# Kernel optimization log

Measured on AMD Instinct MI355X. Metric: run time of the kernel, lower is better.

The kernel has to match this reference:

```python
import jax, jax.numpy as jnp
import numpy as np

N = 50000
E = 600000
D_IN = 128
D_OUT = 128


def setup_inputs() -> dict:
    key = jax.random.key(0)
    k1, k2, k3 = jax.random.split(key, 3)
    x = jax.random.normal(k1, (N, D_IN), dtype=jnp.float32)
    edge_index = jax.random.randint(k2, (2, E), 0, N, dtype=jnp.int64)
    W = jax.random.normal(k3, (D_IN, D_OUT), dtype=jnp.float32) / np.sqrt(D_IN)
    b = jnp.zeros((D_OUT,), dtype=jnp.float32)
    return {"x": x, "edge_index": edge_index, "W": W, "b": b}


def reference(x, edge_index, W, b):
    n = x.shape[0]
    # add self-loops (PyG GCNConv default add_self_loops=True)
    loop = jnp.arange(n, dtype=edge_index.dtype)
    src = jnp.concatenate([edge_index[0], loop])  # message sources
    dst = jnp.concatenate([edge_index[1], loop])  # aggregation targets

    # linear transform first (small GEMM), then normalized aggregation
    h = x @ W  # [N, D_OUT]

    ones = jnp.ones(src.shape[0], dtype=x.dtype)
    deg = jax.ops.segment_sum(ones, dst, num_segments=n)  # in-degree incl. self-loop
    dis = jnp.where(deg > 0, jax.lax.rsqrt(jnp.maximum(deg, 1.0)), 0.0)
    norm = dis[src] * dis[dst]  # [E+N]

    msg = h[src] * norm[:, None]  # gather + scale, memory-bound
    out = jax.ops.segment_sum(msg, dst, num_segments=n)  # scatter-add
    return out + b
```

## Files before the change

kernel.cpp:

```cpp
#include <hip/hip_runtime.h>

#define D 128
#define CAP 1024
#define NBMAX 1024
#define EPB 4096

typedef short bf16x8 __attribute__((ext_vector_type(8)));
typedef float f32x4 __attribute__((ext_vector_type(4)));

__device__ __forceinline__ unsigned bf16_rne(float f) {
    unsigned u = __float_as_uint(f);
    unsigned r = u + 0x7FFFu + ((u >> 16) & 1u);
    return r >> 16;
}

__device__ __forceinline__ void bf16_split(float f, short& hi, short& lo) {
    unsigned h = bf16_rne(f);
    float hf = __uint_as_float(h << 16);
    hi = (short)h;
    lo = (short)bf16_rne(f - hf);
}

__device__ __forceinline__ unsigned pk2(float lo, float hi) {
    return bf16_rne(lo) | (bf16_rne(hi) << 16);
}

__device__ __forceinline__ float lo16(unsigned u) { return __uint_as_float(u << 16); }
__device__ __forceinline__ float hi16(unsigned u) { return __uint_as_float(u & 0xFFFF0000u); }

__global__ void deg_kernel(const int* __restrict__ ei, int* __restrict__ deg, int E) {
    int e = blockIdx.x * blockDim.x + threadIdx.x;
    if (e < E) atomicAdd(&deg[ei[E + e]], 1);
}

__global__ void dis_kernel(const int* __restrict__ deg, float* __restrict__ dis, int n) {
    int i = blockIdx.x * blockDim.x + threadIdx.x;
    if (i < n) dis[i] = rsqrtf((float)(deg[i] + 1));
}

__global__ void wprep_kernel(const float* __restrict__ W, short* __restrict__ wh,
                             short* __restrict__ wl) {
    const int t = blockIdx.x * 256 + threadIdx.x;
    if (t >= 8 * 4 * 64) return;
    const int lane = t & 63;
    const int ks = (t >> 6) & 3;
    const int nt = t >> 8;
    const int nn = nt * 16 + (lane & 15);
    const int kbase = ks * 32 + (lane >> 4) * 8;
#pragma unroll
    for (int j = 0; j < 8; ++j) {
        short hi, lo;
        bf16_split(W[(size_t)(kbase + j) * D + nn], hi, lo);
        wh[(size_t)t * 8 + j] = hi;
        wl[(size_t)t * 8 + j] = lo;
    }
}

__global__ __launch_bounds__(256) void fused_bin_gemm(
        const int* __restrict__ ei, unsigned* __restrict__ bins, int* __restrict__ bcnt,
        int E, int NB, int nbin,
        const float* __restrict__ x, const short* __restrict__ wh,
        const short* __restrict__ wl, const float* __restrict__ dis,
        unsigned* __restrict__ g, int n) {
    __shared__ unsigned staged[EPB];
    __shared__ unsigned short bmap[EPB];
    __shared__ int loff[NBMAX + 1];
    __shared__ int lpos[NBMAX];
    __shared__ int lbase[NBMAX];
    __shared__ int wsum[4];
    const int tid = threadIdx.x;
    const int lane = tid & 63, wid = tid >> 6;

    if ((int)blockIdx.x < nbin) {
        const int base = blockIdx.x * EPB;

        for (int i = tid; i < NBMAX; i += 256) lpos[i] = 0;
        __syncthreads();

        int eb[EPB / 256]; unsigned ev[EPB / 256];
#pragma unroll
        for (int r = 0; r < EPB / 256; ++r) {
            const int idx = base + r * 256 + tid;
            int bkt = -1; unsigned ent = 0;
            if (idx < E) {
                const int s = ei[idx];
                const int d = ei[E + idx];
                bkt = d >> 6;
                ent = (unsigned)s | ((unsigned)(d & 63) << 26);
                atomicAdd(&lpos[bkt], 1);
            }
            eb[r] = bkt; ev[r] = ent;
        }
        __syncthreads();

        {
            const int i0 = tid * 4;
            const int c0 = lpos[i0], c1 = lpos[i0 + 1], c2 = lpos[i0 + 2], c3 = lpos[i0 + 3];
            const int s = c0 + c1 + c2 + c3;
            int sc = s;
#pragma unroll
            for (int o = 1; o < 64; o <<= 1) {
                int t = __shfl_up(sc, o, 64);
                if (lane >= o) sc += t;
            }
            if (lane == 63) wsum[wid] = sc;
            __syncthreads();
            int woff = 0;
#pragma unroll
            for (int w = 0; w < 4; ++w) if (w < wid) woff += wsum[w];
            const int excl = woff + sc - s;
            loff[i0] = excl;
            loff[i0 + 1] = excl + c0;
            loff[i0 + 2] = excl + c0 + c1;
            loff[i0 + 3] = excl + c0 + c1 + c2;
            if (tid == 255) loff[NBMAX] = excl + s;
        }
        __syncthreads();

        for (int i = tid; i < NBMAX; i += 256) {
            const int cnt = loff[i + 1] - loff[i];
            lpos[i] = loff[i];
            lbase[i] = (cnt > 0 && i < NB) ? atomicAdd(&bcnt[i], cnt) : 0;
        }
        __syncthreads();

#pragma unroll
        for (int r = 0; r < EPB / 256; ++r) {
            if (eb[r] >= 0) {
                const int p = atomicAdd(&lpos[eb[r]], 1);
                staged[p] = ev[r];
                bmap[p] = (unsigned short)eb[r];
            }
        }
        __syncthreads();

        const int total = loff[NBMAX];
        for (int slot = tid; slot < total; slot += 256) {
            const int b = bmap[slot];
            const int rel = lbase[b] + (slot - loff[b]);
            if (rel < CAP) bins[(size_t)b * CAP + rel] = staged[slot];
        }
    } else {
        const int bid = (int)blockIdx.x - nbin;
        const int m = lane & 15;
        const int quad = lane >> 4;
        const int row0 = bid * 64 + wid * 16;
        const float* xr = x + (size_t)min(row0 + m, n - 1) * D;

        f32x4 acc[8];
#pragma unroll
        for (int nt = 0; nt < 8; ++nt) acc[nt] = (f32x4){0.f, 0.f, 0.f, 0.f};

#pragma unroll
        for (int ks = 0; ks < 4; ++ks) {
            const float4 xa = *(const float4*)&xr[ks * 32 + quad * 8];
            const float4 xb = *(const float4*)&xr[ks * 32 + quad * 8 + 4];
            bf16x8 ah;
            ah[0] = (short)bf16_rne(xa.x);
            ah[1] = (short)bf16_rne(xa.y);
            ah[2] = (short)bf16_rne(xa.z);
            ah[3] = (short)bf16_rne(xa.w);
            ah[4] = (short)bf16_rne(xb.x);
            ah[5] = (short)bf16_rne(xb.y);
            ah[6] = (short)bf16_rne(xb.z);
            ah[7] = (short)bf16_rne(xb.w);
#pragma unroll
            for (int nt = 0; nt < 8; ++nt) {
                const size_t fo = ((size_t)(nt * 4 + ks) * 64 + lane) * 8;
                const bf16x8 bh = *(const bf16x8*)&wh[fo];
                const bf16x8 bl = *(const bf16x8*)&wl[fo];
                acc[nt] = __builtin_amdgcn_mfma_f32_16x16x32_bf16(ah, bh, acc[nt], 0, 0, 0);
                acc[nt] = __builtin_amdgcn_mfma_f32_16x16x32_bf16(ah, bl, acc[nt], 0, 0, 0);
            }
        }

#pragma unroll
        for (int reg = 0; reg < 4; ++reg) {
            const int rr = row0 + quad * 4 + reg;
            if (rr < n) {
                const float dv = dis[rr];
                unsigned* gr = &g[(size_t)rr * 64 + m];
#pragma unroll
                for (int t = 0; t < 4; ++t)
                    gr[16 * t] = pk2(acc[t][reg] * dv, acc[t + 4][reg] * dv);
            }
        }
    }
}

__global__ __launch_bounds__(256) void sortdis_kernel(unsigned* __restrict__ bins,
                                                      const int* __restrict__ bcnt,
                                                      int* __restrict__ node_off, int n) {
    __shared__ unsigned stage[CAP];
    __shared__ unsigned sorted[CAP];
    __shared__ int hist[64], off[65], pos[64];
    const int b = blockIdx.x;
    const int tid = threadIdx.x;
    const int cnt = min(bcnt[b], CAP);
    if (tid < 64) hist[tid] = 0;
    __syncthreads();
    for (int i = tid; i < cnt; i += 256) {
        const unsigned e = bins[(size_t)b * CAP + i];
        stage[i] = e;
        atomicAdd(&hist[e >> 26], 1);
    }
    __syncthreads();
    if (tid < 64) {
        const int v = hist[tid];
        int sc = v;
#pragma unroll
        for (int o = 1; o < 64; o <<= 1) {
            int t = __shfl_up(sc, o, 64);
            if (tid >= o) sc += t;
        }
        off[tid] = sc - v;
        pos[tid] = sc - v;
        if (tid == 63) off[64] = sc;
    }
    __syncthreads();
    for (int i = tid; i < cnt; i += 256) {
        const unsigned e = stage[i];
        const int p = atomicAdd(&pos[e >> 26], 1);
        sorted[p] = e;
    }
    __syncthreads();
    for (int i = tid; i < cnt; i += 256) bins[(size_t)b * CAP + i] = sorted[i];
    if (tid < 65) node_off[b * 65 + tid] = off[tid];
}

__global__ __launch_bounds__(256) void ngather_kernel(const unsigned* __restrict__ bins,
                                                      const int* __restrict__ node_off,
                                                      const float* __restrict__ dis,
                                                      const unsigned* __restrict__ g,
                                                      const float* __restrict__ bvec,
                                                      float* __restrict__ out, int n) {
    const int node = (blockIdx.x * 256 + threadIdx.x) >> 6;
    const int lane = threadIdx.x & 63;
    if (node >= n) return;
    const int b = node >> 6, j = node & 63;
    const int e0 = node_off[b * 65 + j];
    const int e1 = node_off[b * 65 + j + 1];
    const unsigned* bb = bins + (size_t)b * CAP;

    float a0 = 0.f, a1 = 0.f;
    float p0 = 0.f, p1 = 0.f;
    float q0 = 0.f, q1 = 0.f;
    float r0 = 0.f, r1 = 0.f;

    for (int pos = e0; pos < e1; pos += 64) {
        const int mm = min(64, e1 - pos);
        int ent = 0;
        if (lane < mm) ent = (int)bb[pos + lane];
        for (int t = 0; t < mm; t += 16) {
            const int k = mm - t;
            int ss[16];
#pragma unroll
            for (int i = 0; i < 16; ++i)
                ss[i] = __shfl(ent, min(t + i, mm - 1), 64) & 0x03FFFFFF;
            unsigned uu[16];
#pragma unroll
            for (int i = 0; i < 16; ++i)
                uu[i] = g[(size_t)ss[i] * 64 + lane];
#pragma unroll
            for (int i = 0; i < 16; ++i)
                if (i >= k) uu[i] = 0u;
#pragma unroll
            for (int i = 0; i < 16; i += 4) {
                a0 += lo16(uu[i]);     a1 += hi16(uu[i]);
                p0 += lo16(uu[i + 1]); p1 += hi16(uu[i + 1]);
                q0 += lo16(uu[i + 2]); q1 += hi16(uu[i + 2]);
                r0 += lo16(uu[i + 3]); r1 += hi16(uu[i + 3]);
            }
        }
    }
    const unsigned us = g[(size_t)node * 64 + lane];
    a0 += lo16(us) + p0 + q0 + r0;
    a1 += hi16(us) + p1 + q1 + r1;
    const float dv = dis[node];
    out[(size_t)node * D + lane]      = fmaf(dv, a0, bvec[lane]);
    out[(size_t)node * D + lane + 64] = fmaf(dv, a1, bvec[lane + 64]);
}

extern "C" void kernel_launch(void* const* d_in, const int* in_sizes, int n_in,
                              void* d_out, int out_size, void* d_ws, size_t ws_size,
                              hipStream_t stream) {
    const float* x  = (const float*)d_in[0];
    const int*   ei = (const int*)d_in[1];
    const float* W  = (const float*)d_in[2];
    const float* b  = (const float*)d_in[3];
    float* out = (float*)d_out;

    const int n = in_sizes[0] / D;
    const int E = in_sizes[1] / 2;
    const int NB = (n + 63) >> 6;
    const int nbin = (E + EPB - 1) / EPB;

    char* ws = (char*)d_ws;
    size_t off = 0;
    unsigned* g    = (unsigned*)(ws + off); off += (size_t)n * 64 * sizeof(unsigned);
    float*    dis  = (float*)(ws + off);    off += (size_t)n * sizeof(float);
    unsigned* bins = (unsigned*)(ws + off); off += (size_t)NB * CAP * sizeof(unsigned);
    int*      deg  = (int*)(ws + off);      off += (size_t)n * sizeof(int);
    int*      bcnt = (int*)(ws + off);      off += (size_t)NB * sizeof(int);
    int*  node_off = (int*)(ws + off);      off += (size_t)NB * 65 * sizeof(int);
    short*    wh   = (short*)(ws + off);    off += 8 * 4 * 64 * 8 * sizeof(short);
    short*    wl   = (short*)(ws + off);    off += 8 * 4 * 64 * 8 * sizeof(short);

    hipMemsetAsync(deg, 0, ((size_t)n + NB) * sizeof(int), stream);

    deg_kernel<<<(E + 255) / 256, 256, 0, stream>>>(ei, deg, E);
    dis_kernel<<<(n + 255) / 256, 256, 0, stream>>>(deg, dis, n);
    wprep_kernel<<<8, 256, 0, stream>>>(W, wh, wl);
    fused_bin_gemm<<<nbin + (n + 63) / 64, 256, 0, stream>>>(
        ei, bins, bcnt, E, NB, nbin, x, wh, wl, dis, g, n);
    sortdis_kernel<<<NB, 256, 0, stream>>>(bins, bcnt, node_off, n);
    ngather_kernel<<<(n + 3) / 4, 256, 0, stream>>>(bins, node_off, dis, g, b, out, n);
}
```

Measured before the change: 161.2 us.

## Derive degrees from sorted bin histograms and apply source norm in gather

Drops the separate degree atomic and rsqrt kernels. Normalization factors are now computed from the per-node histogram already built in the sort kernel. Because dis is no longer known when the GEMM writes h, the source-side scaling moves into the gather loop: each edge's dis[src] is loaded and shuffled alongside the index, and the accumulation uses FMAs. This removes two launches and an atomic pass over all edges. In exchange it adds an extra random dis load per edge and more shuffles in the gather, and the degree count is capped by the bin capacity.

After: 133.7 us. 1.21x faster.

```diff
diff --git a/kernel.cpp b/kernel.cpp
--- a/kernel.cpp
+++ b/kernel.cpp
@@ -27,16 +27,6 @@
 
 __device__ __forceinline__ float lo16(unsigned u) { return __uint_as_float(u << 16); }
 __device__ __forceinline__ float hi16(unsigned u) { return __uint_as_float(u & 0xFFFF0000u); }
-
-__global__ void deg_kernel(const int* __restrict__ ei, int* __restrict__ deg, int E) {
-    int e = blockIdx.x * blockDim.x + threadIdx.x;
-    if (e < E) atomicAdd(&deg[ei[E + e]], 1);
-}
-
-__global__ void dis_kernel(const int* __restrict__ deg, float* __restrict__ dis, int n) {
-    int i = blockIdx.x * blockDim.x + threadIdx.x;
-    if (i < n) dis[i] = rsqrtf((float)(deg[i] + 1));
-}
 
 __global__ void wprep_kernel(const float* __restrict__ W, short* __restrict__ wh,
                              short* __restrict__ wl) {
@@ -60,8 +50,7 @@
         const int* __restrict__ ei, unsigned* __restrict__ bins, int* __restrict__ bcnt,
         int E, int NB, int nbin,
         const float* __restrict__ x, const short* __restrict__ wh,
-        const short* __restrict__ wl, const float* __restrict__ dis,
-        unsigned* __restrict__ g, int n) {
+        const short* __restrict__ wl, unsigned* __restrict__ g, int n) {
     __shared__ unsigned staged[EPB];
     __shared__ unsigned short bmap[EPB];
     __shared__ int loff[NBMAX + 1];
@@ -178,11 +167,10 @@
         for (int reg = 0; reg < 4; ++reg) {
             const int rr = row0 + quad * 4 + reg;
             if (rr < n) {
-                const float dv = dis[rr];
                 unsigned* gr = &g[(size_t)rr * 64 + m];
 #pragma unroll
                 for (int t = 0; t < 4; ++t)
-                    gr[16 * t] = pk2(acc[t][reg] * dv, acc[t + 4][reg] * dv);
+                    gr[16 * t] = pk2(acc[t][reg], acc[t + 4][reg]);
             }
         }
     }
@@ -190,7 +178,8 @@
 
 __global__ __launch_bounds__(256) void sortdis_kernel(unsigned* __restrict__ bins,
                                                       const int* __restrict__ bcnt,
-                                                      int* __restrict__ node_off, int n) {
+                                                      int* __restrict__ node_off,
+                                                      float* __restrict__ dis, int n) {
     __shared__ unsigned stage[CAP];
     __shared__ unsigned sorted[CAP];
     __shared__ int hist[64], off[65], pos[64];
@@ -226,6 +215,10 @@
     __syncthreads();
     for (int i = tid; i < cnt; i += 256) bins[(size_t)b * CAP + i] = sorted[i];
     if (tid < 65) node_off[b * 65 + tid] = off[tid];
+    if (tid < 64) {
+        const int node = b * 64 + tid;
+        if (node < n) dis[node] = rsqrtf((float)(hist[tid] + 1));
+    }
 }
 
 __global__ __launch_bounds__(256) void ngather_kernel(const unsigned* __restrict__ bins,
@@ -250,33 +243,44 @@
     for (int pos = e0; pos < e1; pos += 64) {
         const int mm = min(64, e1 - pos);
         int ent = 0;
-        if (lane < mm) ent = (int)bb[pos + lane];
+        float dvl = 0.f;
+        if (lane < mm) {
+            ent = (int)bb[pos + lane];
+            dvl = dis[ent & 0x03FFFFFF];
+        }
         for (int t = 0; t < mm; t += 16) {
             const int k = mm - t;
-            int ss[16];
+            int ss[16]; float nrm[16];
+#pragma unroll
+            for (int i = 0; i < 16; ++i) {
+                const int idx = min(t + i, mm - 1);
+                ss[i] = __shfl(ent, idx, 64) & 0x03FFFFFF;
+                nrm[i] = __shfl(dvl, idx, 64);
+            }
 #pragma unroll
             for (int i = 0; i < 16; ++i)
-                ss[i] = __shfl(ent, min(t + i, mm - 1), 64) & 0x03FFFFFF;
+                if (i >= k) nrm[i] = 0.f;
             unsigned uu[16];
 #pragma unroll
             for (int i = 0; i < 16; ++i)
                 uu[i] = g[(size_t)ss[i] * 64 + lane];
 #pragma unroll
-            for (int i = 0; i < 16; ++i)
-                if (i >= k) uu[i] = 0u;
-#pragma unroll
             for (int i = 0; i < 16; i += 4) {
-                a0 += lo16(uu[i]);     a1 += hi16(uu[i]);
-                p0 += lo16(uu[i + 1]); p1 += hi16(uu[i + 1]);
-                q0 += lo16(uu[i + 2]); q1 += hi16(uu[i + 2]);
-                r0 += lo16(uu[i + 3]); r1 += hi16(uu[i + 3]);
-            }
-        }
-    }
+                a0 = fmaf(nrm[i],     lo16(uu[i]),     a0);
+                a1 = fmaf(nrm[i],     hi16(uu[i]),     a1);
+                p0 = fmaf(nrm[i + 1], lo16(uu[i + 1]), p0);
+                p1 = fmaf(nrm[i + 1], hi16(uu[i + 1]), p1);
+                q0 = fmaf(nrm[i + 2], lo16(uu[i + 2]), q0);
+                q1 = fmaf(nrm[i + 2], hi16(uu[i + 2]), q1);
+                r0 = fmaf(nrm[i + 3], lo16(uu[i + 3]), r0);
+                r1 = fmaf(nrm[i + 3], hi16(uu[i + 3]), r1);
+            }
+        }
+    }
+    const float dv = dis[node];
     const unsigned us = g[(size_t)node * 64 + lane];
-    a0 += lo16(us) + p0 + q0 + r0;
-    a1 += hi16(us) + p1 + q1 + r1;
-    const float dv = dis[node];
+    a0 = fmaf(dv, lo16(us), a0 + p0 + q0 + r0);
+    a1 = fmaf(dv, hi16(us), a1 + p1 + q1 + r1);
     out[(size_t)node * D + lane]      = fmaf(dv, a0, bvec[lane]);
     out[(size_t)node * D + lane + 64] = fmaf(dv, a1, bvec[lane + 64]);
 }
@@ -300,19 +304,16 @@
     unsigned* g    = (unsigned*)(ws + off); off += (size_t)n * 64 * sizeof(unsigned);
     float*    dis  = (float*)(ws + off);    off += (size_t)n * sizeof(float);
     unsigned* bins = (unsigned*)(ws + off); off += (size_t)NB * CAP * sizeof(unsigned);
-    int*      deg  = (int*)(ws + off);      off += (size_t)n * sizeof(int);
     int*      bcnt = (int*)(ws + off);      off += (size_t)NB * sizeof(int);
     int*  node_off = (int*)(ws + off);      off += (size_t)NB * 65 * sizeof(int);
     short*    wh   = (short*)(ws + off);    off += 8 * 4 * 64 * 8 * sizeof(short);
     short*    wl   = (short*)(ws + off);    off += 8 * 4 * 64 * 8 * sizeof(short);
 
-    hipMemsetAsync(deg, 0, ((size_t)n + NB) * sizeof(int), stream);
-
-    deg_kernel<<<(E + 255) / 256, 256, 0, stream>>>(ei, deg, E);
-    dis_kernel<<<(n + 255) / 256, 256, 0, stream>>>(deg, dis, n);
+    hipMemsetAsync(bcnt, 0, (size_t)NB * sizeof(int), stream);
+
     wprep_kernel<<<8, 256, 0, stream>>>(W, wh, wl);
     fused_bin_gemm<<<nbin + (n + 63) / 64, 256, 0, stream>>>(
-        ei, bins, bcnt, E, NB, nbin, x, wh, wl, dis, g, n);
-    sortdis_kernel<<<NB, 256, 0, stream>>>(bins, bcnt, node_off, n);
+        ei, bins, bcnt, E, NB, nbin, x, wh, wl, g, n);
+    sortdis_kernel<<<NB, 256, 0, stream>>>(bins, bcnt, node_off, dis, n);
     ngather_kernel<<<(n + 3) / 4, 256, 0, stream>>>(bins, node_off, dis, g, b, out, n);
 }
```
